# Optimization experiments

Measured on AMD Instinct MI355X. Metric: run time of the kernel, lower is better.

The kernel has to match this reference:

```python
import jax, jax.numpy as jnp
import numpy as np

N_SEGMENTS = 512  # number of superpoint segments (range of sptids)


def setup_inputs() -> dict:
    key = jax.random.key(0)
    k1, k2, k3, k4 = jax.random.split(key, 4)
    n, m, c = 32768, 16384, 21
    points = jax.random.normal(k1, (n, 3), dtype=jnp.float32)
    scores = jax.random.normal(k2, (n, c), dtype=jnp.float32)
    d_points = jax.random.normal(k3, (m, 3), dtype=jnp.float32)
    sptids = jax.random.randint(k4, (m,), 0, N_SEGMENTS, dtype=jnp.int32)
    return {"points": points, "scores": scores, "d_points": d_points, "sptids": sptids}


def reference(points, scores, d_points, sptids):
    # --- brute-force nearest neighbor for ALL downsampled points at once ---
    # squared euclidean distance; argmin is identical to torch.cdist's argmin
    d2 = (jnp.sum(d_points * d_points, axis=1, keepdims=True)
          + jnp.sum(points * points, axis=1)[None, :]
          - 2.0 * (d_points @ points.T))          # [m, n]
    nn_idx = jnp.argmin(d2, axis=1)               # [m]
    gathered = scores[nn_idx]                     # [m, C] == assign_features output

    # --- per-segment mean of gathered scores, then argmax -> segment label ---
    seg_sum = jax.ops.segment_sum(gathered, sptids, num_segments=N_SEGMENTS)  # [S, C]
    counts = jax.ops.segment_sum(jnp.ones(sptids.shape, gathered.dtype), sptids,
                                 num_segments=N_SEGMENTS)                      # [S]
    seg_mean = seg_sum / jnp.maximum(counts, 1.0)[:, None]
    seg_labels = jnp.argmax(seg_mean, axis=1)     # [S]
    labels = seg_labels[sptids][:, None].astype(jnp.int32)  # [m, 1], original index order

    # torch.cat of seg_points over sorted unique ids == stable sort of d_points by sptid
    order = jnp.argsort(sptids, stable=True)
    new_points = d_points[order]                  # [m, 3]
    return new_points, labels
```

## Files before the change

kernel.cpp:

```cpp
#include <hip/hip_runtime.h>
#include <cfloat>
#include <cstdint>

#define NSEG 512
#define C 21
#define PPB 512
#define EPS_PICK 1e-3f
#define SLACK 1.5e-4f

typedef _Float16 half8 __attribute__((ext_vector_type(8)));
typedef float f32x16 __attribute__((ext_vector_type(16)));

__global__ __launch_bounds__(256, 4)
void k1_mfma_scatter(const float* __restrict__ pts, const float* __restrict__ dpts,
                     const int* __restrict__ sptids,
                     float4* __restrict__ pts4, float* __restrict__ pbvT,
                     unsigned* __restrict__ auxT,
                     int* __restrict__ segbase, int* __restrict__ sorted_orig,
                     float* __restrict__ out, int n, int m, int NCH)
{
    __shared__ half8 lbuf[1024];
    const int bid = blockIdx.x, t = threadIdx.x;

    if (bid < NCH) {
        int sb = bid;
        int* Hb   = (int*)lbuf;
        int* Ht   = Hb + NSEG;
        int* pair = Ht + NSEG;
        int* segs = pair + 256;
        Hb[t] = 0; Hb[t + 256] = 0; Ht[t] = 0; Ht[t + 256] = 0;
        __syncthreads();
        int before = sb * 256;
        for (int idx = t; idx < m; idx += 256) {
            int s = sptids[idx];
            atomicAdd(&Ht[s], 1);
            if (idx < before) atomicAdd(&Hb[s], 1);
        }
        __syncthreads();
        int e0 = Ht[2 * t], e1 = Ht[2 * t + 1];
        int v = e0 + e1;
        pair[t] = v;
        __syncthreads();
        for (int off = 1; off < 256; off <<= 1) {
            int add = (t >= off) ? pair[t - off] : 0;
            __syncthreads();
            v += add; pair[t] = v;
            __syncthreads();
        }
        int prev = (t > 0) ? pair[t - 1] : 0;
        int b0 = prev, b1 = prev + e0;
        if (sb == 0) { segbase[2 * t] = b0; segbase[2 * t + 1] = b1; }
        int hb0 = Hb[2 * t], hb1 = Hb[2 * t + 1];
        __syncthreads();
        Hb[2 * t] = b0 + hb0;
        Hb[2 * t + 1] = b1 + hb1;
        int i = sb * 256 + t;
        segs[t] = (i < m) ? sptids[i] : -1;
        __syncthreads();
        if (i < m) {
            int seg = segs[t];
            int rank = 0;
            for (int j = 0; j < t; j++) rank += (segs[j] == seg) ? 1 : 0;
            int pos = Hb[seg] + rank;
            out[pos * 3 + 0] = dpts[i * 3 + 0];
            out[pos * 3 + 1] = dpts[i * 3 + 1];
            out[pos * 3 + 2] = dpts[i * 3 + 2];
            sorted_orig[pos] = i;
        }
        return;
    }

    const int b2 = bid - NCH;
    const int qb = b2 & 31, pc = b2 >> 5;
    const int wave = t >> 6, lane = t & 63;
    const int g = lane >> 5, col = lane & 31;

    half8 bq[4];
#pragma unroll
    for (int k = 0; k < 4; k++) {
        int q = (qb * 16 + wave * 4 + k) * 32 + col;
        float b0 = dpts[q * 3 + 0], b1 = dpts[q * 3 + 1], b2c = dpts[q * 3 + 2];
        _Float16 bh0 = (_Float16)b0; _Float16 bl0 = (_Float16)(b0 - (float)bh0);
        _Float16 bh1 = (_Float16)b1; _Float16 bl1 = (_Float16)(b1 - (float)bh1);
        _Float16 bh2 = (_Float16)b2c; _Float16 bl2 = (_Float16)(b2c - (float)bh2);
        const _Float16 one = (_Float16)1.f, zz = (_Float16)0.f;
        half8 g0 = {bh0, bl0, bh0, bh1, bl1, bh1, bh2, bl2};
        half8 g1 = {bh2, one, one, zz, zz, zz, zz, zz};
        bq[k] = g ? g1 : g0;
    }

#pragma unroll
    for (int half = 0; half < 2; half++) {
        int j = half * 256 + t;
        int i = pc * PPB + j;
        float x = pts[i * 3 + 0], y = pts[i * 3 + 1], z = pts[i * 3 + 2];
        if (qb == 0)
            pts4[i] = make_float4(x, y, z, fmaf(x, x, fmaf(y, y, z * z)));
        float a0 = -2.f * x, a1 = -2.f * y, a2 = -2.f * z;
        _Float16 ah0 = (_Float16)a0; _Float16 al0 = (_Float16)(a0 - (float)ah0);
        _Float16 ah1 = (_Float16)a1; _Float16 al1 = (_Float16)(a1 - (float)ah1);
        _Float16 ah2 = (_Float16)a2; _Float16 al2 = (_Float16)(a2 - (float)ah2);
        double ps = (double)x * x + (double)y * y + (double)z * z;
        _Float16 s0 = (_Float16)(float)ps;
        double r1 = ps - (double)(float)s0;
        _Float16 s1 = (_Float16)(float)r1;
        half8 g0 = {ah0, ah0, al0, ah1, ah1, al1, ah2, ah2};
        half8 g1 = {al2, s0, s1, (_Float16)0.f, (_Float16)0.f,
                    (_Float16)0.f, (_Float16)0.f, (_Float16)0.f};
        int base = (j >> 5) * 64 + (j & 31) * 2;
        lbuf[base + 0] = g0;
        lbuf[base + 1] = g1;
    }
    __syncthreads();

    float run1[4], run2[4];
    int ttix[4];
#pragma unroll
    for (int k = 0; k < 4; k++) { run1[k] = FLT_MAX; run2[k] = FLT_MAX; ttix[k] = 0; }
    const f32x16 zero = {0.f,0.f,0.f,0.f,0.f,0.f,0.f,0.f,0.f,0.f,0.f,0.f,0.f,0.f,0.f,0.f};
    const int aoff = col * 2 + g;

#pragma unroll 4
    for (int tt = 0; tt < 16; tt++) {
        half8 a = lbuf[tt * 64 + aoff];
        f32x16 c0 = __builtin_amdgcn_mfma_f32_32x32x16_f16(a, bq[0], zero, 0, 0, 0);
        f32x16 c1 = __builtin_amdgcn_mfma_f32_32x32x16_f16(a, bq[1], zero, 0, 0, 0);
        f32x16 c2 = __builtin_amdgcn_mfma_f32_32x32x16_f16(a, bq[2], zero, 0, 0, 0);
        f32x16 c3 = __builtin_amdgcn_mfma_f32_32x32x16_f16(a, bq[3], zero, 0, 0, 0);
#define FOLD(cc, kk)  { \
        float v = fminf(fminf(cc[0], cc[1]), cc[2]);   \
        v = fminf(fminf(v, cc[3]), cc[4]);             \
        v = fminf(fminf(v, cc[5]), cc[6]);             \
        v = fminf(fminf(v, cc[7]), cc[8]);             \
        v = fminf(fminf(v, cc[9]), cc[10]);            \
        v = fminf(fminf(v, cc[11]), cc[12]);           \
        v = fminf(fminf(v, cc[13]), cc[14]);           \
        v = fminf(v, cc[15]);                          \
        float nr2 = fminf(run2[kk], fmaxf(v, run1[kk])); \
        if (v < run1[kk]) { ttix[kk] = tt; run1[kk] = v; } \
        run2[kk] = nr2; }
        FOLD(c0, 0) FOLD(c1, 1) FOLD(c2, 2) FOLD(c3, 3)
#undef FOLD
    }

#pragma unroll
    for (int k = 0; k < 4; k++) {
        float o1 = __shfl_xor(run1[k], 32, 64);
        float o2 = __shfl_xor(run2[k], 32, 64);
        int   ot = __shfl_xor(ttix[k], 32, 64);
        float lo1 = (lane < 32) ? run1[k] : o1;  int loT = (lane < 32) ? ttix[k] : ot;
        float lo2 = (lane < 32) ? run2[k] : o2;
        float hi1 = (lane < 32) ? o1 : run1[k];  int hiT = (lane < 32) ? ot : ttix[k];
        float hi2 = (lane < 32) ? o2 : run2[k];
        float r1c = fminf(lo1, hi1);
        int Tstar = (lo1 <= hi1) ? loT : hiT;
        float cl = (loT != Tstar) ? lo1 : lo2;
        float ch = (hiT != Tstar) ? hi1 : hi2;
        float L = fminf(cl, ch);
        if (lane < 32) {
            size_t qi = (size_t)(qb * 512 + wave * 128 + k * 32 + lane) * 64 + pc;
            pbvT[qi] = r1c;
            auxT[qi] = (__float_as_uint(L) & ~0xFu) | (unsigned)Tstar;
        }
    }
}

__global__ __launch_bounds__(1024)
void k2_seg_pick(const float4* __restrict__ pts4, const float* __restrict__ dpts,
                 const float* __restrict__ scores, const float* __restrict__ pbvT,
                 const unsigned* __restrict__ auxT,
                 const int* __restrict__ segbase, const int* __restrict__ sorted_orig,
                 float* __restrict__ out, int n, int m)
{
    __shared__ double wsum[16][C];
    __shared__ double total[C];
    __shared__ float lab;
    const int t = threadIdx.x, wave = t >> 6, lane = t & 63;
    const int s = blockIdx.x;
    const int base = segbase[s];
    const int end  = (s == NSEG - 1) ? m : segbase[s + 1];

    double acc = 0.0;
    for (int j = base + wave; j < end; j += 16) {
        int q = sorted_orig[j];
        float myv = pbvT[(size_t)q * 64 + lane];
        float g1 = myv;
#pragma unroll
        for (int off = 1; off < 64; off <<= 1) g1 = fminf(g1, __shfl_xor(g1, off, 64));
        float thr = g1 + EPS_PICK;
        unsigned long long msk = __ballot(myv <= thr);

        float fx = dpts[q * 3 + 0], fy = dpts[q * 3 + 1], fz = dpts[q * 3 + 2];
        float fm2x = -2.f * fx, fm2y = -2.f * fy, fm2z = -2.f * fz;
        double m2x = -2.0 * (double)fx, m2y = -2.0 * (double)fy, m2z = -2.0 * (double)fz;
        double best = 1e308; int bi = 0x7fffffff;
        while (msk) {
            int pc = __builtin_ctzll(msk); msk &= msk - 1;
            unsigned au = auxT[(size_t)q * 64 + pc];
            float L = __uint_as_float(au & ~0xFu);
            int Ts = (int)(au & 0xFu);
            if (L > thr + SLACK) {
                if (lane < 32) {
                    int i = pc * PPB + Ts * 32 + lane;
                    if (i < n) {
                        float4 p = pts4[i];
                        float v = fmaf(p.x, fm2x, fmaf(p.y, fm2y, fmaf(p.z, fm2z, p.w)));
                        if (v <= thr) {
                            double ps = (double)p.x * p.x + (double)p.y * p.y + (double)p.z * p.z;
                            double dv = fma((double)p.x, m2x, fma((double)p.y, m2y,
                                        fma((double)p.z, m2z, ps)));
                            if (dv < best || (dv == best && i < bi)) { best = dv; bi = i; }
                        }
                    }
                }
            } else {
                int pbase = pc * PPB + lane;
#pragma unroll
                for (int r2 = 0; r2 < PPB / 64; r2++) {
                    int i = pbase + r2 * 64;
                    if (i < n) {
                        float4 p = pts4[i];
                        float v = fmaf(p.x, fm2x, fmaf(p.y, fm2y, fmaf(p.z, fm2z, p.w)));
                        if (v <= thr) {
                            double ps = (double)p.x * p.x + (double)p.y * p.y + (double)p.z * p.z;
                            double dv = fma((double)p.x, m2x, fma((double)p.y, m2y,
                                        fma((double)p.z, m2z, ps)));
                            if (dv < best || (dv == best && i < bi)) { best = dv; bi = i; }
                        }
                    }
                }
            }
        }
#pragma unroll
        for (int off = 32; off; off >>= 1) {
            double ov = __shfl_down(best, off, 64);
            int oi = __shfl_down(bi, off, 64);
            if (ov < best || (ov == best && oi < bi)) { best = ov; bi = oi; }
        }
        int bi0 = __shfl(bi, 0, 64);
        if (lane < C)
            acc += (double)scores[(size_t)bi0 * C + lane];
    }
    if (lane < C) wsum[wave][lane] = acc;
    __syncthreads();
    if (t < C) {
        double tv = 0.0;
#pragma unroll
        for (int w = 0; w < 16; w++) tv += wsum[w][t];
        total[t] = tv;
    }
    __syncthreads();
    if (t == 0) {
        double bv = total[0]; int best = 0;
        for (int c = 1; c < C; c++)
            if (total[c] > bv) { bv = total[c]; best = c; }
        lab = (float)best;
    }
    __syncthreads();
    float fb = lab;
    for (int j = base + t; j < end; j += 1024)
        out[(size_t)m * 3 + sorted_orig[j]] = fb;
}

extern "C" void kernel_launch(void* const* d_in, const int* in_sizes, int n_in,
                              void* d_out, int out_size, void* d_ws, size_t ws_size,
                              hipStream_t stream) {
    const float* points = (const float*)d_in[0];
    const float* scores = (const float*)d_in[1];
    const float* dpts   = (const float*)d_in[2];
    const int*   sptids = (const int*)d_in[3];

    int n = in_sizes[0] / 3;
    int m = in_sizes[2] / 3;
    int NCH   = (m + 255) / 256;
    int QB    = (m + 511) / 512;
    int PCg   = (n + 511) / 512;
    int MFMAB = QB * PCg;

    char* ws = (char*)d_ws;
    float4*   pts4        = (float4*)ws;    ws += (size_t)n * sizeof(float4);
    float*    pbvT        = (float*)ws;     ws += (size_t)m * 64 * sizeof(float);
    unsigned* auxT        = (unsigned*)ws;  ws += (size_t)m * 64 * sizeof(unsigned);
    int*      segbase     = (int*)ws;       ws += (size_t)NSEG * sizeof(int);
    int*      sorted_orig = (int*)ws;       ws += (size_t)m * sizeof(int);

    k1_mfma_scatter<<<NCH + MFMAB, 256, 0, stream>>>(points, dpts, sptids,
                                                     pts4, pbvT, auxT, segbase,
                                                     sorted_orig, (float*)d_out, n, m, NCH);
    k2_seg_pick<<<NSEG, 1024, 0, stream>>>(pts4, dpts, scores, pbvT, auxT,
                                           segbase, sorted_orig, (float*)d_out, n, m);
}
```

Baseline: 47.08 us.

## Split segment pick into per-query NN kernel and per-segment reduction kernel

The fused per-segment kernel, which ran one block per segment with waves looping over that segment's queries, is replaced by two kernels. The first assigns one wave per query to refine the nearest neighbour and writes its index to a new workspace array. The second assigns one wave per segment to sum the gathered scores in registers, take the argmax and scatter the labels. This is meant to remove load imbalance from uneven segment sizes and give the refinement step more parallelism, at the cost of one extra launch and a global round trip for the indices.

```diff
diff --git a/kernel.cpp b/kernel.cpp
--- a/kernel.cpp
+++ b/kernel.cpp
@@ -165,100 +165,103 @@
     }
 }
 
-__global__ __launch_bounds__(1024)
-void k2_seg_pick(const float4* __restrict__ pts4, const float* __restrict__ dpts,
-                 const float* __restrict__ scores, const float* __restrict__ pbvT,
-                 const unsigned* __restrict__ auxT,
-                 const int* __restrict__ segbase, const int* __restrict__ sorted_orig,
-                 float* __restrict__ out, int n, int m)
+__global__ __launch_bounds__(512)
+void pick(const float4* __restrict__ pts4, const float* __restrict__ dpts,
+          const float* __restrict__ pbvT, const unsigned* __restrict__ auxT,
+          int* __restrict__ nn_idx, int n, int m)
 {
-    __shared__ double wsum[16][C];
-    __shared__ double total[C];
-    __shared__ float lab;
-    const int t = threadIdx.x, wave = t >> 6, lane = t & 63;
-    const int s = blockIdx.x;
-    const int base = segbase[s];
-    const int end  = (s == NSEG - 1) ? m : segbase[s + 1];
-
-    double acc = 0.0;
-    for (int j = base + wave; j < end; j += 16) {
-        int q = sorted_orig[j];
-        float myv = pbvT[(size_t)q * 64 + lane];
-        float g1 = myv;
-#pragma unroll
-        for (int off = 1; off < 64; off <<= 1) g1 = fminf(g1, __shfl_xor(g1, off, 64));
-        float thr = g1 + EPS_PICK;
-        unsigned long long msk = __ballot(myv <= thr);
-
-        float fx = dpts[q * 3 + 0], fy = dpts[q * 3 + 1], fz = dpts[q * 3 + 2];
-        float fm2x = -2.f * fx, fm2y = -2.f * fy, fm2z = -2.f * fz;
-        double m2x = -2.0 * (double)fx, m2y = -2.0 * (double)fy, m2z = -2.0 * (double)fz;
-        double best = 1e308; int bi = 0x7fffffff;
-        while (msk) {
-            int pc = __builtin_ctzll(msk); msk &= msk - 1;
-            unsigned au = auxT[(size_t)q * 64 + pc];
-            float L = __uint_as_float(au & ~0xFu);
-            int Ts = (int)(au & 0xFu);
-            if (L > thr + SLACK) {
-                if (lane < 32) {
-                    int i = pc * PPB + Ts * 32 + lane;
-                    if (i < n) {
-                        float4 p = pts4[i];
-                        float v = fmaf(p.x, fm2x, fmaf(p.y, fm2y, fmaf(p.z, fm2z, p.w)));
-                        if (v <= thr) {
-                            double ps = (double)p.x * p.x + (double)p.y * p.y + (double)p.z * p.z;
-                            double dv = fma((double)p.x, m2x, fma((double)p.y, m2y,
-                                        fma((double)p.z, m2z, ps)));
-                            if (dv < best || (dv == best && i < bi)) { best = dv; bi = i; }
-                        }
-                    }
-                }
-            } else {
-                int pbase = pc * PPB + lane;
-#pragma unroll
-                for (int r2 = 0; r2 < PPB / 64; r2++) {
-                    int i = pbase + r2 * 64;
-                    if (i < n) {
-                        float4 p = pts4[i];
-                        float v = fmaf(p.x, fm2x, fmaf(p.y, fm2y, fmaf(p.z, fm2z, p.w)));
-                        if (v <= thr) {
-                            double ps = (double)p.x * p.x + (double)p.y * p.y + (double)p.z * p.z;
-                            double dv = fma((double)p.x, m2x, fma((double)p.y, m2y,
-                                        fma((double)p.z, m2z, ps)));
-                            if (dv < best || (dv == best && i < bi)) { best = dv; bi = i; }
-                        }
+    int wave = threadIdx.x >> 6, lane = threadIdx.x & 63;
+    int q = blockIdx.x * 8 + wave;
+    if (q >= m) return;
+
+    float fx = dpts[q * 3 + 0], fy = dpts[q * 3 + 1], fz = dpts[q * 3 + 2];
+    float myv = pbvT[(size_t)q * 64 + lane];
+    float g1 = myv;
+#pragma unroll
+    for (int off = 1; off < 64; off <<= 1) g1 = fminf(g1, __shfl_xor(g1, off, 64));
+    float thr = g1 + EPS_PICK;
+    unsigned long long msk = __ballot(myv <= thr);
+
+    float fm2x = -2.f * fx, fm2y = -2.f * fy, fm2z = -2.f * fz;
+    double m2x = -2.0 * (double)fx, m2y = -2.0 * (double)fy, m2z = -2.0 * (double)fz;
+    double best = 1e308; int bi = 0x7fffffff;
+    while (msk) {
+        int pc = __builtin_ctzll(msk); msk &= msk - 1;
+        unsigned au = auxT[(size_t)q * 64 + pc];
+        float L = __uint_as_float(au & ~0xFu);
+        int Ts = (int)(au & 0xFu);
+        if (L > thr + SLACK) {
+            if (lane < 32) {
+                int i = pc * PPB + Ts * 32 + lane;
+                if (i < n) {
+                    float4 p = pts4[i];
+                    float v = fmaf(p.x, fm2x, fmaf(p.y, fm2y, fmaf(p.z, fm2z, p.w)));
+                    if (v <= thr) {
+                        double ps = (double)p.x * p.x + (double)p.y * p.y + (double)p.z * p.z;
+                        double dv = fma((double)p.x, m2x, fma((double)p.y, m2y,
+                                    fma((double)p.z, m2z, ps)));
+                        if (dv < best || (dv == best && i < bi)) { best = dv; bi = i; }
                     }
                 }
             }
-        }
-#pragma unroll
-        for (int off = 32; off; off >>= 1) {
-            double ov = __shfl_down(best, off, 64);
-            int oi = __shfl_down(bi, off, 64);
-            if (ov < best || (ov == best && oi < bi)) { best = ov; bi = oi; }
-        }
-        int bi0 = __shfl(bi, 0, 64);
-        if (lane < C)
-            acc += (double)scores[(size_t)bi0 * C + lane];
-    }
-    if (lane < C) wsum[wave][lane] = acc;
-    __syncthreads();
-    if (t < C) {
-        double tv = 0.0;
-#pragma unroll
-        for (int w = 0; w < 16; w++) tv += wsum[w][t];
-        total[t] = tv;
-    }
-    __syncthreads();
-    if (t == 0) {
-        double bv = total[0]; int best = 0;
+        } else {
+            int pbase = pc * PPB + lane;
+#pragma unroll
+            for (int r2 = 0; r2 < PPB / 64; r2++) {
+                int i = pbase + r2 * 64;
+                if (i < n) {
+                    float4 p = pts4[i];
+                    float v = fmaf(p.x, fm2x, fmaf(p.y, fm2y, fmaf(p.z, fm2z, p.w)));
+                    if (v <= thr) {
+                        double ps = (double)p.x * p.x + (double)p.y * p.y + (double)p.z * p.z;
+                        double dv = fma((double)p.x, m2x, fma((double)p.y, m2y,
+                                    fma((double)p.z, m2z, ps)));
+                        if (dv < best || (dv == best && i < bi)) { best = dv; bi = i; }
+                    }
+                }
+            }
+        }
+    }
+#pragma unroll
+    for (int off = 32; off; off >>= 1) {
+        double ov = __shfl_down(best, off, 64);
+        int oi = __shfl_down(bi, off, 64);
+        if (ov < best || (ov == best && oi < bi)) { best = ov; bi = oi; }
+    }
+    if (lane == 0) nn_idx[q] = bi;
+}
+
+__global__ __launch_bounds__(512)
+void seg_final(const int* __restrict__ segbase, const int* __restrict__ sorted_orig,
+               const int* __restrict__ nn_idx, const float* __restrict__ scores,
+               float* __restrict__ out, int m)
+{
+    int wave = threadIdx.x >> 6, lane = threadIdx.x & 63;
+    int s = blockIdx.x * 8 + wave;
+    if (s >= NSEG) return;
+    int base = segbase[s];
+    int end  = (s == NSEG - 1) ? m : segbase[s + 1];
+    double acc[C];
+#pragma unroll
+    for (int c = 0; c < C; c++) acc[c] = 0.0;
+    for (int j = base + lane; j < end; j += 64) {
+        const float* sp = scores + (size_t)nn_idx[sorted_orig[j]] * C;
+#pragma unroll
+        for (int c = 0; c < C; c++) acc[c] += (double)sp[c];
+    }
+#pragma unroll
+    for (int c = 0; c < C; c++) {
+        for (int off = 32; off; off >>= 1) acc[c] += __shfl_down(acc[c], off, 64);
+    }
+    int best = 0;
+    if (lane == 0) {
+        double bv = acc[0];
         for (int c = 1; c < C; c++)
-            if (total[c] > bv) { bv = total[c]; best = c; }
-        lab = (float)best;
-    }
-    __syncthreads();
-    float fb = lab;
-    for (int j = base + t; j < end; j += 1024)
+            if (acc[c] > bv) { bv = acc[c]; best = c; }
+    }
+    best = __shfl(best, 0, 64);
+    float fb = (float)best;
+    for (int j = base + lane; j < end; j += 64)
         out[(size_t)m * 3 + sorted_orig[j]] = fb;
 }
 
@@ -281,12 +284,14 @@
     float4*   pts4        = (float4*)ws;    ws += (size_t)n * sizeof(float4);
     float*    pbvT        = (float*)ws;     ws += (size_t)m * 64 * sizeof(float);
     unsigned* auxT        = (unsigned*)ws;  ws += (size_t)m * 64 * sizeof(unsigned);
+    int*      nn_idx      = (int*)ws;       ws += (size_t)m * sizeof(int);
     int*      segbase     = (int*)ws;       ws += (size_t)NSEG * sizeof(int);
     int*      sorted_orig = (int*)ws;       ws += (size_t)m * sizeof(int);
 
     k1_mfma_scatter<<<NCH + MFMAB, 256, 0, stream>>>(points, dpts, sptids,
                                                      pts4, pbvT, auxT, segbase,
                                                      sorted_orig, (float*)d_out, n, m, NCH);
-    k2_seg_pick<<<NSEG, 1024, 0, stream>>>(pts4, dpts, scores, pbvT, auxT,
-                                           segbase, sorted_orig, (float*)d_out, n, m);
-}
+    pick<<<(m + 7) / 8, 512, 0, stream>>>(pts4, dpts, pbvT, auxT, nn_idx, n, m);
+    seg_final<<<NSEG / 8, 512, 0, stream>>>(segbase, sorted_orig, nn_idx, scores,
+                                            (float*)d_out, m);
+}
```

Result: slower. 51.08 us (+8.5%).
